# Performance work log

Hardware: AMD Instinct MI355X
Metric: run time of the kernel (lower is better)

## Reference

```python
import jax, jax.numpy as jnp
import numpy as np

N = 25000      # nodes
E = 250000     # edges (per graph)
D_IN = 256     # input feature dim
H = 4          # heads (both stages)
D = 64         # per-head out dim (hidden_size1 == hidden_size2)
NEG_SLOPE = 0.2  # DGL GATConv default leaky_relu slope


def gat_layer(x, W, al, ar, b, src, dst):
    # x: [N, F_in]; W: [F_in, H*D]; al, ar: [H, D]; b: [H*D]
    feat = (x @ W).reshape(N, H, D)                       # [N,H,D]
    el = jnp.einsum('nhd,hd->nh', feat, al)               # [N,H]
    er = jnp.einsum('nhd,hd->nh', feat, ar)               # [N,H]
    e = jax.nn.leaky_relu(el[src] + er[dst], NEG_SLOPE)   # [E,H]
    # edge softmax over incoming edges of each dst node
    m = jax.ops.segment_max(e, dst, num_segments=N)       # [N,H]
    a = jnp.exp(e - m[dst])                               # [E,H]
    s = jax.ops.segment_sum(a, dst, num_segments=N)       # [N,H]
    alpha = a / s[dst]                                    # [E,H]
    out = jax.ops.segment_sum(alpha[:, :, None] * feat[src], dst, num_segments=N)  # [N,H,D]
    return jax.nn.relu(out + b.reshape(1, H, D))


def dot_score(h, u, v):
    # u_dot_v over last dim: h [N,H,D] -> score [E,H,1]
    return jnp.sum(h[u] * h[v], axis=-1, keepdims=True)


def setup_inputs() -> dict:
    key = jax.random.key(0)
    ks = jax.random.split(key, 16)
    x = jax.random.normal(ks[0], (N, D_IN), dtype=jnp.float32)
    src = jax.random.randint(ks[1], (E,), 0, N, dtype=jnp.int32)
    dst = jax.random.randint(ks[2], (E,), 0, N, dtype=jnp.int32)
    neg_src = jax.random.randint(ks[3], (E,), 0, N, dtype=jnp.int32)
    neg_dst = jax.random.randint(ks[4], (E,), 0, N, dtype=jnp.int32)
    sc = 0.1
    params = {}
    fin = D_IN
    for i in range(3):
        k = 5 + 3 * i
        params[f'W{i+1}'] = sc * jax.random.normal(ks[k], (fin, H * D), dtype=jnp.float32)
        params[f'al{i+1}'] = sc * jax.random.normal(ks[k + 1], (H, D), dtype=jnp.float32)
        params[f'ar{i+1}'] = sc * jax.random.normal(ks[k + 2], (H, D), dtype=jnp.float32)
        params[f'b{i+1}'] = jnp.zeros((H * D,), dtype=jnp.float32)
        fin = H * D
    return dict(x=x, src=src, dst=dst, neg_src=neg_src, neg_dst=neg_dst, **params)


def reference(x, src, dst, neg_src, neg_dst,
              W1, al1, ar1, b1, W2, al2, ar2, b2, W3, al3, ar3, b3):
    h = gat_layer(x, W1, al1, ar1, b1, src, dst)
    h = gat_layer(h.reshape(N, -1), W2, al2, ar2, b2, src, dst)
    h = gat_layer(h.reshape(N, -1), W3, al3, ar3, b3, src, dst)  # [N,H,D]
    return dot_score(h, src, dst), dot_score(h, neg_src, neg_dst)
```

## Files before the change

### kernel.cpp

```cpp
#include <hip/hip_runtime.h>
#include <hip/hip_bf16.h>
#include <math.h>

#define N_NODES 25000
#define N_EDGES 250000
#define NH 4
#define F 256
#define NEG_SLOPE 0.2f

typedef float  f32x4 __attribute__((ext_vector_type(4)));
typedef short  s16x8 __attribute__((ext_vector_type(8)));
typedef ushort u16x8 __attribute__((ext_vector_type(8)));

__device__ inline ushort f2bf(float f) {
    uint u = __float_as_uint(f);
    u += 0x7FFF + ((u >> 16) & 1);
    return (ushort)(u >> 16);
}
__device__ inline float bf2f(ushort s) { return __uint_as_float(((uint)s) << 16); }

__global__ __launch_bounds__(256) void k_cast(const float* __restrict__ x,
                                              ushort* __restrict__ xb) {
    int i = blockIdx.x * blockDim.x + threadIdx.x;
    if (i * 4 >= N_NODES * F) return;
    float4 v = *(const float4*)&x[i * 4];
    ushort4 o;
    o.x = f2bf(v.x); o.y = f2bf(v.y); o.z = f2bf(v.z); o.w = f2bf(v.w);
    *(ushort4*)&xb[i * 4] = o;
}

__global__ void k_degree(const int* __restrict__ dst, int* deg) {
    int e = blockIdx.x * blockDim.x + threadIdx.x;
    if (e < N_EDGES) atomicAdd(&deg[dst[e]], 1);
}

__global__ __launch_bounds__(1024) void k_scan(const int* __restrict__ deg, int* rowptr) {
    __shared__ int sums[1024];
    const int CH = 25;
    int t = threadIdx.x;
    int base = t * CH;
    int s = 0;
    for (int i = 0; i < CH; ++i) {
        int idx = base + i;
        if (idx < N_NODES) s += deg[idx];
    }
    sums[t] = s;
    __syncthreads();
    for (int off = 1; off < 1024; off <<= 1) {
        int v = (t >= off) ? sums[t - off] : 0;
        __syncthreads();
        sums[t] += v;
        __syncthreads();
    }
    int prefix = (t == 0) ? 0 : sums[t - 1];
    for (int i = 0; i < CH; ++i) {
        int idx = base + i;
        if (idx < N_NODES) {
            rowptr[idx] = prefix;
            prefix += deg[idx];
        }
    }
    if (t == 1023) rowptr[N_NODES] = prefix;
}

__global__ void k_bucket(const int* __restrict__ src, const int* __restrict__ dst,
                         const int* __restrict__ rowptr, int* cursor,
                         int* esrc, int* edst, int* eid) {
    int e = blockIdx.x * blockDim.x + threadIdx.x;
    if (e >= N_EDGES) return;
    int d = dst[e];
    int p = atomicAdd(&cursor[d], 1);
    int slot = rowptr[d] + p;
    esrc[slot] = src[e];
    edst[slot] = d;
    eid[slot]  = e;
}

__global__ __launch_bounds__(256) void k_wprep(const float* __restrict__ W,
        short* __restrict__ Hi) {
    __shared__ float T[64][65];
    int bk = (blockIdx.x & 3) * 64;
    int bn = (blockIdx.x >> 2) * 64;
    int t = threadIdx.x;
    int r = t >> 6, c = t & 63;
    #pragma unroll
    for (int i = 0; i < 64; i += 4)
        T[r + i][c] = W[(bk + r + i) * 256 + bn + c];
    __syncthreads();
    #pragma unroll
    for (int i = 0; i < 64; i += 4) {
        float w = T[c][r + i];
        Hi[(bn + r + i) * 256 + bk + c] = (short)f2bf(w);
    }
}

__global__ __launch_bounds__(256) void k_gemm(const ushort* __restrict__ A,
        const short* __restrict__ Wt,
        const float* __restrict__ alv, const float* __restrict__ arv,
        ushort* __restrict__ Cbf, float* __restrict__ el, float* __restrict__ er,
        int M) {
    __shared__ short As[2][64][32];
    __shared__ short Ws[2][256][32];
    int tid = threadIdx.x;
    int w = tid >> 6, l = tid & 63;
    int row0 = blockIdx.x * 64;

    f32x4 acc[4][4];
    #pragma unroll
    for (int i = 0; i < 4; ++i)
        #pragma unroll
        for (int j = 0; j < 4; ++j)
            acc[i][j] = (f32x4){0.f, 0.f, 0.f, 0.f};

    const int sr = tid >> 2;
    const int sk = tid & 3;
    const int sa = sk ^ ((sr >> 1) & 3);

    s16x8 aReg;
    s16x8 whr[4];

    {
        int gr = row0 + sr;
        aReg = (s16x8){0,0,0,0,0,0,0,0};
        if (gr < M) aReg = *(const s16x8*)&A[gr * 256 + sk * 8];
        #pragma unroll
        for (int r = 0; r < 4; ++r) {
            int n = sr + 64 * r;
            whr[r] = *(const s16x8*)&Wt[n * 256 + sk * 8];
        }
        *(s16x8*)&As[0][sr][sa * 8] = aReg;
        #pragma unroll
        for (int r = 0; r < 4; ++r) {
            int n = sr + 64 * r;
            int sw = sk ^ ((n >> 1) & 3);
            *(s16x8*)&Ws[0][n][sw * 8] = whr[r];
        }
    }
    __syncthreads();

    const int r16 = l & 15, kg = l >> 4;
    for (int c = 0; c < 8; ++c) {
        const int b = c & 1;
        if (c < 7) {
            int kc = (c + 1) * 32;
            int gr = row0 + sr;
            aReg = (s16x8){0,0,0,0,0,0,0,0};
            if (gr < M) aReg = *(const s16x8*)&A[gr * 256 + kc + sk * 8];
            #pragma unroll
            for (int r = 0; r < 4; ++r) {
                int n = sr + 64 * r;
                whr[r] = *(const s16x8*)&Wt[n * 256 + kc + sk * 8];
            }
        }
        s16x8 ah[4], bh[4];
        #pragma unroll
        for (int i = 0; i < 4; ++i) {
            int r = i * 16 + r16;
            int s = (kg ^ ((r >> 1) & 3)) * 8;
            ah[i] = *(const s16x8*)&As[b][r][s];
        }
        #pragma unroll
        for (int j = 0; j < 4; ++j) {
            int cc = w * 64 + j * 16 + r16;
            int s = (kg ^ ((cc >> 1) & 3)) * 8;
            bh[j] = *(const s16x8*)&Ws[b][cc][s];
        }
        #pragma unroll
        for (int i = 0; i < 4; ++i)
            #pragma unroll
            for (int j = 0; j < 4; ++j)
                acc[i][j] = __builtin_amdgcn_mfma_f32_16x16x32_bf16(ah[i], bh[j], acc[i][j], 0, 0, 0);
        if (c < 7) {
            *(s16x8*)&As[b ^ 1][sr][sa * 8] = aReg;
            #pragma unroll
            for (int r = 0; r < 4; ++r) {
                int n = sr + 64 * r;
                int sw = sk ^ ((n >> 1) & 3);
                *(s16x8*)&Ws[b ^ 1][n][sw * 8] = whr[r];
            }
        }
        __syncthreads();
    }

    float ac4[4], rc4[4];
    #pragma unroll
    for (int j = 0; j < 4; ++j) {
        ac4[j] = alv[w * 64 + j * 16 + r16];
        rc4[j] = arv[w * 64 + j * 16 + r16];
    }
    #pragma unroll
    for (int i = 0; i < 4; ++i) {
        #pragma unroll
        for (int q = 0; q < 4; ++q) {
            int gr = row0 + i * 16 + kg * 4 + q;
            float pel = 0.f, per = 0.f;
            #pragma unroll
            for (int j = 0; j < 4; ++j) {
                float v = acc[i][j][q];
                pel += v * ac4[j];
                per += v * rc4[j];
            }
            pel += __shfl_xor(pel, 1);  per += __shfl_xor(per, 1);
            pel += __shfl_xor(pel, 2);  per += __shfl_xor(per, 2);
            pel += __shfl_xor(pel, 4);  per += __shfl_xor(per, 4);
            pel += __shfl_xor(pel, 8);  per += __shfl_xor(per, 8);
            if (r16 == 0 && gr < M) {
                el[gr * NH + w] = pel;
                er[gr * NH + w] = per;
            }
        }
    }
    #pragma unroll
    for (int i = 0; i < 4; ++i)
        #pragma unroll
        for (int j = 0; j < 4; ++j) {
            int cc = w * 64 + j * 16 + r16;
            #pragma unroll
            for (int q = 0; q < 4; ++q) {
                int gr = row0 + i * 16 + kg * 4 + q;
                if (gr < M) Cbf[gr * 256 + cc] = f2bf(acc[i][j][q]);
            }
        }
}

__global__ __launch_bounds__(256) void k_node(const ushort* __restrict__ featbf,
        const float* __restrict__ el, const float* __restrict__ er,
        const int* __restrict__ rowptr, const int* __restrict__ esrc,
        const float* __restrict__ bias,
        ushort* __restrict__ hbf) {
    int t = threadIdx.x;
    int n = blockIdx.x * 2 + (t >> 7);
    if (n >= N_NODES) return;
    int tt = t & 127;
    int c0 = tt * 2;
    int h = tt >> 5;
    float ern = er[n * NH + h];
    int r0 = rowptr[n], r1 = rowptr[n + 1];
    float acc0 = 0.f, acc1 = 0.f, S = 0.f;
    int i = r0;
    for (; i + 4 <= r1; i += 4) {
        int s0 = esrc[i], s1 = esrc[i + 1], s2 = esrc[i + 2], s3 = esrc[i + 3];
        uint p0 = *(const uint*)&featbf[s0 * F + c0];
        uint p1 = *(const uint*)&featbf[s1 * F + c0];
        uint p2 = *(const uint*)&featbf[s2 * F + c0];
        uint p3 = *(const uint*)&featbf[s3 * F + c0];
        float e0 = el[s0 * NH + h] + ern;
        float e1 = el[s1 * NH + h] + ern;
        float e2 = el[s2 * NH + h] + ern;
        float e3 = el[s3 * NH + h] + ern;
        e0 = e0 > 0.f ? e0 : NEG_SLOPE * e0;
        e1 = e1 > 0.f ? e1 : NEG_SLOPE * e1;
        e2 = e2 > 0.f ? e2 : NEG_SLOPE * e2;
        e3 = e3 > 0.f ? e3 : NEG_SLOPE * e3;
        float a0 = __expf(e0), a1 = __expf(e1), a2 = __expf(e2), a3 = __expf(e3);
        S += (a0 + a1) + (a2 + a3);
        acc0 += a0 * bf2f((ushort)(p0 & 0xFFFF)) + a1 * bf2f((ushort)(p1 & 0xFFFF))
              + a2 * bf2f((ushort)(p2 & 0xFFFF)) + a3 * bf2f((ushort)(p3 & 0xFFFF));
        acc1 += a0 * bf2f((ushort)(p0 >> 16))    + a1 * bf2f((ushort)(p1 >> 16))
              + a2 * bf2f((ushort)(p2 >> 16))    + a3 * bf2f((ushort)(p3 >> 16));
    }
    for (; i < r1; ++i) {
        int s0 = esrc[i];
        uint p0 = *(const uint*)&featbf[s0 * F + c0];
        float e0 = el[s0 * NH + h] + ern;
        e0 = e0 > 0.f ? e0 : NEG_SLOPE * e0;
        float a0 = __expf(e0);
        S += a0;
        acc0 += a0 * bf2f((ushort)(p0 & 0xFFFF));
        acc1 += a0 * bf2f((ushort)(p0 >> 16));
    }
    float inv = S > 0.f ? 1.f / S : 0.f;
    float o0 = acc0 * inv + bias[c0];
    float o1 = acc1 * inv + bias[c0 + 1];
    o0 = o0 > 0.f ? o0 : 0.f;
    o1 = o1 > 0.f ? o1 : 0.f;
    uint pk = (uint)f2bf(o0) | ((uint)f2bf(o1) << 16);
    *(uint*)&hbf[n * F + c0] = pk;
}

__global__ __launch_bounds__(256) void k_score(const ushort* __restrict__ h,
        const int* __restrict__ esrc, const int* __restrict__ edst,
        const int* __restrict__ eid,
        const int* __restrict__ nsrc, const int* __restrict__ ndst,
        float* __restrict__ out) {
    int g = blockIdx.x * 16 + (threadIdx.x >> 4);
    int sub = threadIdx.x & 15;
    int u, v;
    float* o;
    if (g < N_EDGES) {
        u = esrc[g]; v = edst[g];
        o = out + (size_t)eid[g] * NH;
    } else {
        int e = g - N_EDGES;
        u = nsrc[e]; v = ndst[e];
        o = out + (size_t)(N_EDGES + e) * NH;
    }
    u16x8 a0 = *(const u16x8*)&h[u * F + sub * 16];
    u16x8 a1 = *(const u16x8*)&h[u * F + sub * 16 + 8];
    u16x8 b0 = *(const u16x8*)&h[v * F + sub * 16];
    u16x8 b1 = *(const u16x8*)&h[v * F + sub * 16 + 8];
    float p = 0.f;
    #pragma unroll
    for (int i = 0; i < 8; ++i) {
        p += bf2f(a0[i]) * bf2f(b0[i]);
        p += bf2f(a1[i]) * bf2f(b1[i]);
    }
    p += __shfl_xor(p, 1);
    p += __shfl_xor(p, 2);
    if ((sub & 3) == 0) o[sub >> 2] = p;
}

extern "C" void kernel_launch(void* const* d_in, const int* in_sizes, int n_in,
                              void* d_out, int out_size, void* d_ws, size_t ws_size,
                              hipStream_t stream) {
    const float* x    = (const float*)d_in[0];
    const int* src    = (const int*)d_in[1];
    const int* dst    = (const int*)d_in[2];
    const int* nsrc   = (const int*)d_in[3];
    const int* ndst   = (const int*)d_in[4];
    const float* W[3]  = {(const float*)d_in[5], (const float*)d_in[9],  (const float*)d_in[13]};
    const float* al[3] = {(const float*)d_in[6], (const float*)d_in[10], (const float*)d_in[14]};
    const float* ar[3] = {(const float*)d_in[7], (const float*)d_in[11], (const float*)d_in[15]};
    const float* bs[3] = {(const float*)d_in[8], (const float*)d_in[12], (const float*)d_in[16]};

    char* p = (char*)d_ws;
    auto alloc = [&](size_t bytes) {
        char* r = p;
        p += (bytes + 255) & ~size_t(255);
        return r;
    };
    ushort* xbf    = (ushort*)alloc(sizeof(ushort) * N_NODES * F);
    ushort* featbf = (ushort*)alloc(sizeof(ushort) * N_NODES * F);
    ushort* hA     = (ushort*)alloc(sizeof(ushort) * N_NODES * F);
    ushort* hB     = (ushort*)alloc(sizeof(ushort) * N_NODES * F);
    float* el    = (float*)alloc(sizeof(float) * N_NODES * NH);
    float* er    = (float*)alloc(sizeof(float) * N_NODES * NH);
    int* deg     = (int*)alloc(sizeof(int) * N_NODES);
    int* cursor  = (int*)alloc(sizeof(int) * N_NODES);
    int* rowptr  = (int*)alloc(sizeof(int) * (N_NODES + 1));
    int* esrc    = (int*)alloc(sizeof(int) * N_EDGES);
    int* edst    = (int*)alloc(sizeof(int) * N_EDGES);
    int* eid     = (int*)alloc(sizeof(int) * N_EDGES);
    short* wt[3];
    for (int i = 0; i < 3; ++i)
        wt[i] = (short*)alloc(sizeof(short) * 256 * 256);

    (void)hipMemsetAsync(deg, 0, sizeof(int) * N_NODES, stream);
    (void)hipMemsetAsync(cursor, 0, sizeof(int) * N_NODES, stream);

    int eb = (N_EDGES + 255) / 256;
    k_cast<<<(N_NODES * F / 4 + 255) / 256, 256, 0, stream>>>(x, xbf);
    k_degree<<<eb, 256, 0, stream>>>(dst, deg);
    k_scan<<<1, 1024, 0, stream>>>(deg, rowptr);
    k_bucket<<<eb, 256, 0, stream>>>(src, dst, rowptr, cursor, esrc, edst, eid);
    for (int L = 0; L < 3; ++L)
        k_wprep<<<16, 256, 0, stream>>>(W[L], wt[L]);

    const ushort* in_h = xbf;
    ushort* outs[3] = {hA, hB, hA};
    int gemm_grid = (N_NODES + 63) / 64;
    int node_grid = (N_NODES + 1) / 2;
    for (int L = 0; L < 3; ++L) {
        k_gemm<<<gemm_grid, 256, 0, stream>>>(in_h, wt[L], al[L], ar[L],
                                              featbf, el, er, N_NODES);
        k_node<<<node_grid, 256, 0, stream>>>(featbf, el, er, rowptr, esrc, bs[L], outs[L]);
        in_h = outs[L];
    }
    k_score<<<(2 * N_EDGES) / 16, 256, 0, stream>>>(outs[2], esrc, edst, eid, nsrc, ndst, (float*)d_out);
}
```

Before: 367.9 us.

## Bucket negative edges by dst, halve GEMM tile, widen node aggregation loads

Negative edges now go into the same CSR bucketing as positive edges, keyed by dst, so the score kernel reads both sorted lists with better locality for the v row. The GEMM row tile drops from 64 to 32 rows per block, which doubles the grid at the cost of lower MFMA reuse per W tile load. The node aggregation kernel moves to one 64-lane wave per node: each lane loads 8 bf16 values with 16-byte loads and the two half-waves split the edges, combined at the end with a shuffle. The extra bucketing adds atomics and a longer single-block scan.

```diff
diff --git a/kernel.cpp b/kernel.cpp
--- a/kernel.cpp
+++ b/kernel.cpp
@@ -3,6 +3,7 @@
 #include <math.h>
 
 #define N_NODES 25000
+#define N_TOT   50000
 #define N_EDGES 250000
 #define NH 4
 #define F 256
@@ -29,20 +30,23 @@
     *(ushort4*)&xb[i * 4] = o;
 }
 
-__global__ void k_degree(const int* __restrict__ dst, int* deg) {
+__global__ void k_degree(const int* __restrict__ dst, const int* __restrict__ ndst,
+                         int* deg) {
     int e = blockIdx.x * blockDim.x + threadIdx.x;
-    if (e < N_EDGES) atomicAdd(&deg[dst[e]], 1);
+    if (e >= N_EDGES) return;
+    atomicAdd(&deg[dst[e]], 1);
+    atomicAdd(&deg[N_NODES + ndst[e]], 1);
 }
 
 __global__ __launch_bounds__(1024) void k_scan(const int* __restrict__ deg, int* rowptr) {
     __shared__ int sums[1024];
-    const int CH = 25;
+    const int CH = 49;
     int t = threadIdx.x;
     int base = t * CH;
     int s = 0;
     for (int i = 0; i < CH; ++i) {
         int idx = base + i;
-        if (idx < N_NODES) s += deg[idx];
+        if (idx < N_TOT) s += deg[idx];
     }
     sums[t] = s;
     __syncthreads();
@@ -55,25 +59,36 @@
     int prefix = (t == 0) ? 0 : sums[t - 1];
     for (int i = 0; i < CH; ++i) {
         int idx = base + i;
-        if (idx < N_NODES) {
+        if (idx < N_TOT) {
             rowptr[idx] = prefix;
             prefix += deg[idx];
         }
     }
-    if (t == 1023) rowptr[N_NODES] = prefix;
+    if (t == 1023) rowptr[N_TOT] = prefix;
 }
 
 __global__ void k_bucket(const int* __restrict__ src, const int* __restrict__ dst,
+                         const int* __restrict__ nsrc, const int* __restrict__ ndst,
                          const int* __restrict__ rowptr, int* cursor,
-                         int* esrc, int* edst, int* eid) {
+                         int* cesrc, int* cedst, int* ceid) {
     int e = blockIdx.x * blockDim.x + threadIdx.x;
     if (e >= N_EDGES) return;
-    int d = dst[e];
-    int p = atomicAdd(&cursor[d], 1);
-    int slot = rowptr[d] + p;
-    esrc[slot] = src[e];
-    edst[slot] = d;
-    eid[slot]  = e;
+    {
+        int d = dst[e];
+        int p = atomicAdd(&cursor[d], 1);
+        int slot = rowptr[d] + p;
+        cesrc[slot] = src[e];
+        cedst[slot] = d;
+        ceid[slot]  = e;
+    }
+    {
+        int d = N_NODES + ndst[e];
+        int p = atomicAdd(&cursor[d], 1);
+        int slot = rowptr[d] + p;
+        cesrc[slot] = nsrc[e];
+        cedst[slot] = ndst[e];
+        ceid[slot]  = N_EDGES + e;
+    }
 }
 
 __global__ __launch_bounds__(256) void k_wprep(const float* __restrict__ W,
@@ -99,15 +114,15 @@
         const float* __restrict__ alv, const float* __restrict__ arv,
         ushort* __restrict__ Cbf, float* __restrict__ el, float* __restrict__ er,
         int M) {
-    __shared__ short As[2][64][32];
+    __shared__ short As[2][32][32];
     __shared__ short Ws[2][256][32];
     int tid = threadIdx.x;
     int w = tid >> 6, l = tid & 63;
-    int row0 = blockIdx.x * 64;
-
-    f32x4 acc[4][4];
-    #pragma unroll
-    for (int i = 0; i < 4; ++i)
+    int row0 = blockIdx.x * 32;
+
+    f32x4 acc[2][4];
+    #pragma unroll
+    for (int i = 0; i < 2; ++i)
         #pragma unroll
         for (int j = 0; j < 4; ++j)
             acc[i][j] = (f32x4){0.f, 0.f, 0.f, 0.f};
@@ -120,18 +135,20 @@
     s16x8 whr[4];
 
     {
-        int gr = row0 + sr;
         aReg = (s16x8){0,0,0,0,0,0,0,0};
-        if (gr < M) aReg = *(const s16x8*)&A[gr * 256 + sk * 8];
+        if (tid < 128) {
+            int gr = row0 + sr;
+            if (gr < M) aReg = *(const s16x8*)&A[gr * 256 + sk * 8];
+        }
         #pragma unroll
         for (int r = 0; r < 4; ++r) {
-            int n = sr + 64 * r;
+            int n = (tid >> 2) + 64 * r;
             whr[r] = *(const s16x8*)&Wt[n * 256 + sk * 8];
         }
-        *(s16x8*)&As[0][sr][sa * 8] = aReg;
+        if (tid < 128) *(s16x8*)&As[0][sr][sa * 8] = aReg;
         #pragma unroll
         for (int r = 0; r < 4; ++r) {
-            int n = sr + 64 * r;
+            int n = (tid >> 2) + 64 * r;
             int sw = sk ^ ((n >> 1) & 3);
             *(s16x8*)&Ws[0][n][sw * 8] = whr[r];
         }
@@ -143,18 +160,20 @@
         const int b = c & 1;
         if (c < 7) {
             int kc = (c + 1) * 32;
-            int gr = row0 + sr;
             aReg = (s16x8){0,0,0,0,0,0,0,0};
-            if (gr < M) aReg = *(const s16x8*)&A[gr * 256 + kc + sk * 8];
+            if (tid < 128) {
+                int gr = row0 + sr;
+                if (gr < M) aReg = *(const s16x8*)&A[gr * 256 + kc + sk * 8];
+            }
             #pragma unroll
             for (int r = 0; r < 4; ++r) {
-                int n = sr + 64 * r;
+                int n = (tid >> 2) + 64 * r;
                 whr[r] = *(const s16x8*)&Wt[n * 256 + kc + sk * 8];
             }
         }
-        s16x8 ah[4], bh[4];
-        #pragma unroll
-        for (int i = 0; i < 4; ++i) {
+        s16x8 ah[2], bh[4];
+        #pragma unroll
+        for (int i = 0; i < 2; ++i) {
             int r = i * 16 + r16;
             int s = (kg ^ ((r >> 1) & 3)) * 8;
             ah[i] = *(const s16x8*)&As[b][r][s];
@@ -166,15 +185,15 @@
             bh[j] = *(const s16x8*)&Ws[b][cc][s];
         }
         #pragma unroll
-        for (int i = 0; i < 4; ++i)
+        for (int i = 0; i < 2; ++i)
             #pragma unroll
             for (int j = 0; j < 4; ++j)
                 acc[i][j] = __builtin_amdgcn_mfma_f32_16x16x32_bf16(ah[i], bh[j], acc[i][j], 0, 0, 0);
         if (c < 7) {
-            *(s16x8*)&As[b ^ 1][sr][sa * 8] = aReg;
+            if (tid < 128) *(s16x8*)&As[b ^ 1][sr][sa * 8] = aReg;
             #pragma unroll
             for (int r = 0; r < 4; ++r) {
-                int n = sr + 64 * r;
+                int n = (tid >> 2) + 64 * r;
                 int sw = sk ^ ((n >> 1) & 3);
                 *(s16x8*)&Ws[b ^ 1][n][sw * 8] = whr[r];
             }
@@ -189,7 +208,7 @@
         rc4[j] = arv[w * 64 + j * 16 + r16];
     }
     #pragma unroll
-    for (int i = 0; i < 4; ++i) {
+    for (int i = 0; i < 2; ++i) {
         #pragma unroll
         for (int q = 0; q < 4; ++q) {
             int gr = row0 + i * 16 + kg * 4 + q;
@@ -211,7 +230,7 @@
         }
     }
     #pragma unroll
-    for (int i = 0; i < 4; ++i)
+    for (int i = 0; i < 2; ++i)
         #pragma unroll
         for (int j = 0; j < 4; ++j) {
             int cc = w * 64 + j * 16 + r16;
@@ -225,76 +244,90 @@
 
 __global__ __launch_bounds__(256) void k_node(const ushort* __restrict__ featbf,
         const float* __restrict__ el, const float* __restrict__ er,
-        const int* __restrict__ rowptr, const int* __restrict__ esrc,
+        const int* __restrict__ rowptr, const int* __restrict__ cesrc,
         const float* __restrict__ bias,
         ushort* __restrict__ hbf) {
     int t = threadIdx.x;
-    int n = blockIdx.x * 2 + (t >> 7);
+    int n = blockIdx.x * 4 + (t >> 6);
     if (n >= N_NODES) return;
-    int tt = t & 127;
-    int c0 = tt * 2;
-    int h = tt >> 5;
+    int l = t & 63;
+    int half = l >> 5;
+    int lc = l & 31;
+    int c0 = lc * 8;
+    int h = lc >> 3;
     float ern = er[n * NH + h];
     int r0 = rowptr[n], r1 = rowptr[n + 1];
-    float acc0 = 0.f, acc1 = 0.f, S = 0.f;
-    int i = r0;
-    for (; i + 4 <= r1; i += 4) {
-        int s0 = esrc[i], s1 = esrc[i + 1], s2 = esrc[i + 2], s3 = esrc[i + 3];
-        uint p0 = *(const uint*)&featbf[s0 * F + c0];
-        uint p1 = *(const uint*)&featbf[s1 * F + c0];
-        uint p2 = *(const uint*)&featbf[s2 * F + c0];
-        uint p3 = *(const uint*)&featbf[s3 * F + c0];
+    float S = 0.f;
+    float ac[8] = {0.f, 0.f, 0.f, 0.f, 0.f, 0.f, 0.f, 0.f};
+    int p = r0 + half;
+    for (; p + 2 < r1; p += 4) {
+        int s0 = cesrc[p], s1 = cesrc[p + 2];
+        uint4 q0 = *(const uint4*)&featbf[s0 * F + c0];
+        uint4 q1 = *(const uint4*)&featbf[s1 * F + c0];
         float e0 = el[s0 * NH + h] + ern;
         float e1 = el[s1 * NH + h] + ern;
-        float e2 = el[s2 * NH + h] + ern;
-        float e3 = el[s3 * NH + h] + ern;
         e0 = e0 > 0.f ? e0 : NEG_SLOPE * e0;
         e1 = e1 > 0.f ? e1 : NEG_SLOPE * e1;
-        e2 = e2 > 0.f ? e2 : NEG_SLOPE * e2;
-        e3 = e3 > 0.f ? e3 : NEG_SLOPE * e3;
-        float a0 = __expf(e0), a1 = __expf(e1), a2 = __expf(e2), a3 = __expf(e3);
-        S += (a0 + a1) + (a2 + a3);
-        acc0 += a0 * bf2f((ushort)(p0 & 0xFFFF)) + a1 * bf2f((ushort)(p1 & 0xFFFF))
-              + a2 * bf2f((ushort)(p2 & 0xFFFF)) + a3 * bf2f((ushort)(p3 & 0xFFFF));
-        acc1 += a0 * bf2f((ushort)(p0 >> 16))    + a1 * bf2f((ushort)(p1 >> 16))
-              + a2 * bf2f((ushort)(p2 >> 16))    + a3 * bf2f((ushort)(p3 >> 16));
-    }
-    for (; i < r1; ++i) {
-        int s0 = esrc[i];
-        uint p0 = *(const uint*)&featbf[s0 * F + c0];
+        float a0 = __expf(e0), a1 = __expf(e1);
+        S += a0 + a1;
+        ac[0] += a0 * bf2f((ushort)(q0.x & 0xFFFF)) + a1 * bf2f((ushort)(q1.x & 0xFFFF));
+        ac[1] += a0 * bf2f((ushort)(q0.x >> 16))    + a1 * bf2f((ushort)(q1.x >> 16));
+        ac[2] += a0 * bf2f((ushort)(q0.y & 0xFFFF)) + a1 * bf2f((ushort)(q1.y & 0xFFFF));
+        ac[3] += a0 * bf2f((ushort)(q0.y >> 16))    + a1 * bf2f((ushort)(q1.y >> 16));
+        ac[4] += a0 * bf2f((ushort)(q0.z & 0xFFFF)) + a1 * bf2f((ushort)(q1.z & 0xFFFF));
+        ac[5] += a0 * bf2f((ushort)(q0.z >> 16))    + a1 * bf2f((ushort)(q1.z >> 16));
+        ac[6] += a0 * bf2f((ushort)(q0.w & 0xFFFF)) + a1 * bf2f((ushort)(q1.w & 0xFFFF));
+        ac[7] += a0 * bf2f((ushort)(q0.w >> 16))    + a1 * bf2f((ushort)(q1.w >> 16));
+    }
+    if (p < r1) {
+        int s0 = cesrc[p];
+        uint4 q0 = *(const uint4*)&featbf[s0 * F + c0];
         float e0 = el[s0 * NH + h] + ern;
         e0 = e0 > 0.f ? e0 : NEG_SLOPE * e0;
         float a0 = __expf(e0);
         S += a0;
-        acc0 += a0 * bf2f((ushort)(p0 & 0xFFFF));
-        acc1 += a0 * bf2f((ushort)(p0 >> 16));
-    }
-    float inv = S > 0.f ? 1.f / S : 0.f;
-    float o0 = acc0 * inv + bias[c0];
-    float o1 = acc1 * inv + bias[c0 + 1];
-    o0 = o0 > 0.f ? o0 : 0.f;
-    o1 = o1 > 0.f ? o1 : 0.f;
-    uint pk = (uint)f2bf(o0) | ((uint)f2bf(o1) << 16);
-    *(uint*)&hbf[n * F + c0] = pk;
+        ac[0] += a0 * bf2f((ushort)(q0.x & 0xFFFF));
+        ac[1] += a0 * bf2f((ushort)(q0.x >> 16));
+        ac[2] += a0 * bf2f((ushort)(q0.y & 0xFFFF));
+        ac[3] += a0 * bf2f((ushort)(q0.y >> 16));
+        ac[4] += a0 * bf2f((ushort)(q0.z & 0xFFFF));
+        ac[5] += a0 * bf2f((ushort)(q0.z >> 16));
+        ac[6] += a0 * bf2f((ushort)(q0.w & 0xFFFF));
+        ac[7] += a0 * bf2f((ushort)(q0.w >> 16));
+    }
+    S += __shfl_xor(S, 32);
+    #pragma unroll
+    for (int j = 0; j < 8; ++j) ac[j] += __shfl_xor(ac[j], 32);
+    if (half == 0) {
+        float inv = S > 0.f ? 1.f / S : 0.f;
+        float4 b0 = *(const float4*)&bias[c0];
+        float4 b1 = *(const float4*)&bias[c0 + 4];
+        float o0 = ac[0] * inv + b0.x;  float o1 = ac[1] * inv + b0.y;
+        float o2 = ac[2] * inv + b0.z;  float o3 = ac[3] * inv + b0.w;
+        float o4 = ac[4] * inv + b1.x;  float o5 = ac[5] * inv + b1.y;
+        float o6 = ac[6] * inv + b1.z;  float o7 = ac[7] * inv + b1.w;
+        o0 = o0 > 0.f ? o0 : 0.f;  o1 = o1 > 0.f ? o1 : 0.f;
+        o2 = o2 > 0.f ? o2 : 0.f;  o3 = o3 > 0.f ? o3 : 0.f;
+        o4 = o4 > 0.f ? o4 : 0.f;  o5 = o5 > 0.f ? o5 : 0.f;
+        o6 = o6 > 0.f ? o6 : 0.f;  o7 = o7 > 0.f ? o7 : 0.f;
+        uint4 pk;
+        pk.x = (uint)f2bf(o0) | ((uint)f2bf(o1) << 16);
+        pk.y = (uint)f2bf(o2) | ((uint)f2bf(o3) << 16);
+        pk.z = (uint)f2bf(o4) | ((uint)f2bf(o5) << 16);
+        pk.w = (uint)f2bf(o6) | ((uint)f2bf(o7) << 16);
+        *(uint4*)&hbf[n * F + c0] = pk;
+    }
 }
 
 __global__ __launch_bounds__(256) void k_score(const ushort* __restrict__ h,
-        const int* __restrict__ esrc, const int* __restrict__ edst,
-        const int* __restrict__ eid,
-        const int* __restrict__ nsrc, const int* __restrict__ ndst,
+        const int* __restrict__ cesrc, const int* __restrict__ cedst,
+        const int* __restrict__ ceid,
         float* __restrict__ out) {
     int g = blockIdx.x * 16 + (threadIdx.x >> 4);
     int sub = threadIdx.x & 15;
-    int u, v;
-    float* o;
-    if (g < N_EDGES) {
-        u = esrc[g]; v = edst[g];
-        o = out + (size_t)eid[g] * NH;
-    } else {
-        int e = g - N_EDGES;
-        u = nsrc[e]; v = ndst[e];
-        o = out + (size_t)(N_EDGES + e) * NH;
-    }
+    int u = cesrc[g];
+    int v = cedst[g];
+    float* o = out + (size_t)ceid[g] * NH;
     u16x8 a0 = *(const u16x8*)&h[u * F + sub * 16];
     u16x8 a1 = *(const u16x8*)&h[u * F + sub * 16 + 8];
     u16x8 b0 = *(const u16x8*)&h[v * F + sub * 16];
@@ -335,36 +368,37 @@
     ushort* hB     = (ushort*)alloc(sizeof(ushort) * N_NODES * F);
     float* el    = (float*)alloc(sizeof(float) * N_NODES * NH);
     float* er    = (float*)alloc(sizeof(float) * N_NODES * NH);
-    int* deg     = (int*)alloc(sizeof(int) * N_NODES);
-    int* cursor  = (int*)alloc(sizeof(int) * N_NODES);
-    int* rowptr  = (int*)alloc(sizeof(int) * (N_NODES + 1));
-    int* esrc    = (int*)alloc(sizeof(int) * N_EDGES);
-    int* edst    = (int*)alloc(sizeof(int) * N_EDGES);
-    int* eid     = (int*)alloc(sizeof(int) * N_EDGES);
+    int* deg     = (int*)alloc(sizeof(int) * N_TOT);
+    int* cursor  = (int*)alloc(sizeof(int) * N_TOT);
+    int* rowptr  = (int*)alloc(sizeof(int) * (N_TOT + 1));
+    int* cesrc   = (int*)alloc(sizeof(int) * 2 * N_EDGES);
+    int* cedst   = (int*)alloc(sizeof(int) * 2 * N_EDGES);
+    int* ceid    = (int*)alloc(sizeof(int) * 2 * N_EDGES);
     short* wt[3];
     for (int i = 0; i < 3; ++i)
         wt[i] = (short*)alloc(sizeof(short) * 256 * 256);
 
-    (void)hipMemsetAsync(deg, 0, sizeof(int) * N_NODES, stream);
-    (void)hipMemsetAsync(cursor, 0, sizeof(int) * N_NODES, stream);
+    (void)hipMemsetAsync(deg, 0, sizeof(int) * N_TOT, stream);
+    (void)hipMemsetAsync(cursor, 0, sizeof(int) * N_TOT, stream);
 
     int eb = (N_EDGES + 255) / 256;
     k_cast<<<(N_NODES * F / 4 + 255) / 256, 256, 0, stream>>>(x, xbf);
-    k_degree<<<eb, 256, 0, stream>>>(dst, deg);
+    k_degree<<<eb, 256, 0, stream>>>(dst, ndst, deg);
     k_scan<<<1, 1024, 0, stream>>>(deg, rowptr);
-    k_bucket<<<eb, 256, 0, stream>>>(src, dst, rowptr, cursor, esrc, edst, eid);
+    k_bucket<<<eb, 256, 0, stream>>>(src, dst, nsrc, ndst, rowptr, cursor,
+                                     cesrc, cedst, ceid);
     for (int L = 0; L < 3; ++L)
         k_wprep<<<16, 256, 0, stream>>>(W[L], wt[L]);
 
     const ushort* in_h = xbf;
     ushort* outs[3] = {hA, hB, hA};
-    int gemm_grid = (N_NODES + 63) / 64;
-    int node_grid = (N_NODES + 1) / 2;
+    int gemm_grid = (N_NODES + 31) / 32;
+    int node_grid = (N_NODES + 3) / 4;
     for (int L = 0; L < 3; ++L) {
         k_gemm<<<gemm_grid, 256, 0, stream>>>(in_h, wt[L], al[L], ar[L],
                                               featbf, el, er, N_NODES);
-        k_node<<<node_grid, 256, 0, stream>>>(featbf, el, er, rowptr, esrc, bs[L], outs[L]);
+        k_node<<<node_grid, 256, 0, stream>>>(featbf, el, er, rowptr, cesrc, bs[L], outs[L]);
         in_h = outs[L];
     }
-    k_score<<<(2 * N_EDGES) / 16, 256, 0, stream>>>(outs[2], esrc, edst, eid, nsrc, ndst, (float*)d_out);
-}
+    k_score<<<(2 * N_EDGES) / 16, 256, 0, stream>>>(outs[2], cesrc, cedst, ceid, (float*)d_out);
+}
```

Measured after the change: 414.8 us. +12.8%, slower.
